# Performance work log

Measured on AMD Instinct MI355X. Metric: run time of the kernel, lower is better.

Reference implementation:

```python
import jax, jax.numpy as jnp
import numpy as np

B, T, N, D, R, K, P = 4, 336, 862, 64, 8, 6, 96


def setup_inputs() -> dict:
    key = jax.random.key(0)
    ks = jax.random.split(key, 8)
    s = 0.02
    return {
        "x_enc": jax.random.normal(ks[0], (B, T, N), jnp.float32),
        "W_embed": jax.random.normal(ks[1], (1, D), jnp.float32) * s,
        "b_embed": jnp.zeros((D,), jnp.float32),
        "W1": jax.random.normal(ks[2], (D, R), jnp.float32) * s,
        "W2": jax.random.normal(ks[3], (D, R), jnp.float32) * s,
        "gate": jnp.float32(-4.0),  # gate_init
        "A_prior": jnp.eye(N, dtype=jnp.float32),  # season_gcn_adj_source=identity
        "W_gcn": jax.random.normal(ks[4], (D, D), jnp.float32) * s,
        "g_gcn": jnp.float32(0.5),  # season_gcn gate
        "W_head": jax.random.normal(ks[5], (T * D, P), jnp.float32) * s,
        "b_head": jnp.zeros((P,), jnp.float32),
    }


def _topk_renorm(adj, k):
    # keep top-k entries per row, zero the rest, renormalize rows (matches _sparsify_adj)
    vals = jax.lax.top_k(adj, k)[0]
    thresh = vals[..., -1:]
    mask = (adj >= thresh).astype(adj.dtype)
    masked = adj * mask
    denom = jnp.clip(jnp.sum(masked, axis=-1, keepdims=True), 1e-12, None)
    return masked / denom


def reference(x_enc, W_embed, b_embed, W1, W2, gate, A_prior, W_gcn, g_gcn, W_head, b_head):
    # per-variable, per-timestep value embedding: [B,N,T,D]
    h = x_enc.transpose(0, 2, 1)[..., None] * W_embed[0] + b_embed
    # content-mean node descriptors: [B,N,D]
    z = jnp.mean(h, axis=2)
    # low-rank graph learner -> adjacency logits [B,N,N]
    e1 = z @ W1
    e2 = z @ W2
    logits = jnp.einsum('bnr,bmr->bnm', e1, e2) / jnp.sqrt(jnp.float32(R))
    adj = jax.nn.softmax(logits, axis=-1)
    adj = _topk_renorm(adj, K)  # top-k sparsify + row renorm
    # gated graph mixing over variable nodes
    h_mix = jnp.einsum('bnm,bmtd->bntd', adj, h)
    h = h + jax.nn.sigmoid(gate) * h_mix
    # season GCN: sym-normalized prior adjacency, residual + gate
    deg = jnp.sum(A_prior, axis=-1)
    dinv = jnp.where(deg > 0, 1.0 / jnp.sqrt(deg), 0.0)
    A_hat = A_prior * dinv[:, None] * dinv[None, :]
    h = h + g_gcn * jnp.einsum('nm,bmtd,de->bnte', A_hat, h, W_gcn)
    # forecast head: flatten tokens, project to pred_len per variable
    out = h.reshape(B, N, T * D) @ W_head + b_head  # [B,N,P]
    return out.transpose(0, 2, 1)  # [B,P,N]
```

## Files before the change

kernel.cpp:

```cpp
#include <hip/hip_runtime.h>
#include <math.h>

#define B_ 4
#define T_ 336
#define N_ 862
#define D_ 64
#define R_ 8
#define K_ 6
#define P_ 96
#define NR 896
#define CAP 32
#define NB 864

#define OFF_PC   0
#define OFF_XBAR 192
#define OFF_DINV 3648
#define OFF_WGT  4512
#define OFF_IDX  25248
#define OFF_CNT  45984
#define OFF_CSRV 46848
#define OFF_CSRI 74496
#define OFF_P12  102144
#define OFF_PCP  166656
#define OFF_XPT  231168

__global__ __launch_bounds__(192) void kA_prep(const float* __restrict__ x,
                                               const float* __restrict__ Whead,
                                               const float* __restrict__ We,
                                               const float* __restrict__ be,
                                               const float* __restrict__ gate,
                                               const float* __restrict__ Wgcn,
                                               float* __restrict__ ws) {
  int id = blockIdx.x;
  int tid = threadIdx.x;
  if (id < 336) {
    __shared__ float sW1[64], sW2[64], sCB[64], sWe[64];
    int t = id;
    float g = 1.f / (1.f + expf(-gate[0]));
    if (tid < 64) {
      float a = 0.f;
#pragma unroll 8
      for (int dd = 0; dd < D_; ++dd) a += We[dd] * Wgcn[dd * D_ + tid];
      sW1[tid] = a;
    } else if (tid < 128) {
      int e = tid - 64;
      float a = 0.f;
#pragma unroll 8
      for (int dd = 0; dd < D_; ++dd) a += be[dd] * Wgcn[dd * D_ + e];
      sW2[e] = (1.f + g) * a;
    } else {
      int e = tid - 128;
      sCB[e] = (1.f + g) * be[e];
      sWe[e] = We[e];
    }
    __syncthreads();
    int c = tid, p = c % P_, sel = c / P_;
    const float* cA = sel ? sW1 : sWe;
    const float* cB = sel ? sW2 : sCB;
    const float* wrow = Whead + (size_t)t * D_ * P_ + p;
    float a = 0.f, bacc = 0.f;
#pragma unroll 8
    for (int e = 0; e < D_; ++e) {
      float w = wrow[(size_t)e * P_];
      a = fmaf(cA[e], w, a);
      bacc = fmaf(cB[e], w, bacc);
    }
    ws[OFF_P12 + t * 192 + c] = a;
    ws[OFF_PCP + t * 192 + c] = bacc;
  } else {
    __shared__ float part[192];
    int iq = id - 336;
    int b = iq / 14, ch = iq % 14;
    int lane = tid & 63, tg = tid >> 6;
    int n = ch * 64 + lane;
    float s = 0.f;
    if (n < N_) {
      const float* xp = x + (size_t)(b * T_) * N_ + n;
      for (int t = tg; t < T_; t += 3) s += xp[(size_t)t * N_];
    }
    part[tid] = s;
    __syncthreads();
    if (tg == 0 && n < N_)
      ws[OFF_XBAR + b * NB + n] = part[lane] + part[64 + lane] + part[128 + lane];
  }
}

__global__ __launch_bounds__(192) void kM_mid(const float* __restrict__ x,
                                              const float* __restrict__ A,
                                              const float* __restrict__ W1,
                                              const float* __restrict__ W2,
                                              const float* __restrict__ We,
                                              const float* __restrict__ be,
                                              const float* __restrict__ gate,
                                              float* __restrict__ ws) {
  __shared__ float smem[9984];
  int id = blockIdx.x;
  int tid = threadIdx.x;
  if (id < 216) {
    float* xs = smem;
    float* ps = smem + 768;
    int b = id / 54;
    int n0 = (id % 54) * 16;
    int cq = tid % 48, nq = tid / 48;
    int c0 = cq * 4;
    const float* P = ws + OFF_P12;
    float acc[4][4];
#pragma unroll
    for (int i = 0; i < 4; ++i)
#pragma unroll
      for (int j = 0; j < 4; ++j) acc[i][j] = 0.f;
    int xrow = tid >> 2, xcol4 = tid & 3;
    for (int kc = 0; kc < 7; ++kc) {
      int t0 = kc * 48;
      {
        const float* xr = x + (size_t)(b * T_ + t0 + xrow) * N_;
        if (n0 + 15 < N_) {
          *(float4*)(xs + xrow * 16 + xcol4 * 4) = *(const float4*)(xr + n0 + xcol4 * 4);
        } else {
          float* dst = xs + xrow * 16 + xcol4 * 4;
#pragma unroll
          for (int q = 0; q < 4; ++q) {
            int nn = n0 + xcol4 * 4 + q; if (nn > N_ - 1) nn = N_ - 1;
            dst[q] = xr[nn];
          }
        }
      }
#pragma unroll
      for (int sIdx = 0; sIdx < 12; ++sIdx) {
        int i4 = tid + sIdx * 192;
        int row = i4 / 48, col4 = i4 % 48;
        *(float4*)(ps + row * 192 + col4 * 4) =
            *(const float4*)(P + (size_t)(t0 + row) * 192 + col4 * 4);
      }
      __syncthreads();
#pragma unroll 4
      for (int kk = 0; kk < 48; ++kk) {
        float4 xv = *(const float4*)(xs + kk * 16 + nq * 4);
        float4 pv = *(const float4*)(ps + kk * 192 + c0);
        acc[0][0] = fmaf(pv.x, xv.x, acc[0][0]); acc[0][1] = fmaf(pv.x, xv.y, acc[0][1]);
        acc[0][2] = fmaf(pv.x, xv.z, acc[0][2]); acc[0][3] = fmaf(pv.x, xv.w, acc[0][3]);
        acc[1][0] = fmaf(pv.y, xv.x, acc[1][0]); acc[1][1] = fmaf(pv.y, xv.y, acc[1][1]);
        acc[1][2] = fmaf(pv.y, xv.z, acc[1][2]); acc[1][3] = fmaf(pv.y, xv.w, acc[1][3]);
        acc[2][0] = fmaf(pv.z, xv.x, acc[2][0]); acc[2][1] = fmaf(pv.z, xv.y, acc[2][1]);
        acc[2][2] = fmaf(pv.z, xv.z, acc[2][2]); acc[2][3] = fmaf(pv.z, xv.w, acc[2][3]);
        acc[3][0] = fmaf(pv.w, xv.x, acc[3][0]); acc[3][1] = fmaf(pv.w, xv.y, acc[3][1]);
        acc[3][2] = fmaf(pv.w, xv.z, acc[3][2]); acc[3][3] = fmaf(pv.w, xv.w, acc[3][3]);
      }
      __syncthreads();
    }
#pragma unroll
    for (int cc = 0; cc < 4; ++cc) {
      float4 v;
      v.x = acc[cc][0]; v.y = acc[cc][1]; v.z = acc[cc][2]; v.w = acc[cc][3];
      *(float4*)(ws + OFF_XPT + ((size_t)(b * 192 + c0 + cc)) * NR + n0 + nq * 4) = v;
    }
  } else if (id < 220) {
    __shared__ float s_sc[4][R_];
    __shared__ float s_scal[5];
    __shared__ float selv[12];
    __shared__ int seli[12];
    float* sx = smem;
    float* wkmax = smem + 864;
    float* wkmin = smem + 1728;
    int b = id - 216;
    if (tid < 16) {
      int r = tid & 7, which = tid >> 3;
      const float* W = which ? W2 : W1;
      float a = 0.f, bb = 0.f;
      for (int dd = 0; dd < D_; ++dd) {
        float w = W[dd * R_ + r];
        a += We[dd] * w; bb += be[dd] * w;
      }
      s_sc[which * 2][r] = a; s_sc[which * 2 + 1][r] = bb;
    }
    const float invT = 1.f / (float)T_;
    for (int i = tid; i < NB; i += 192) {
      float v = (i < N_) ? ws[OFF_XBAR + b * NB + i] * invT : 0.f;
      sx[i] = v;
      wkmax[i] = (i < N_) ? v : -3.4e38f;
      wkmin[i] = (i < N_) ? v : 3.4e38f;
    }
    __syncthreads();
    if (tid == 0) {
      float s11 = 0.f, s12 = 0.f, s21 = 0.f, s22 = 0.f;
      for (int r = 0; r < R_; ++r) {
        s11 += s_sc[0][r] * s_sc[2][r];
        s12 += s_sc[0][r] * s_sc[3][r];
        s21 += s_sc[1][r] * s_sc[2][r];
        s22 += s_sc[1][r] * s_sc[3][r];
      }
      s_scal[0] = s11; s_scal[1] = s12; s_scal[2] = s21; s_scal[3] = s22;
      s_scal[4] = 1.f / (1.f + expf(-gate[0]));
    }
    if (tid < 64) {
      int lane = tid;
      for (int r = 0; r < K_; ++r) {
        float bv = -3.4e38f; int bi = 0;
        for (int i = lane; i < N_; i += 64) {
          float v = wkmax[i];
          if (v > bv) { bv = v; bi = i; }
        }
        for (int off = 32; off; off >>= 1) {
          float ov = __shfl_down(bv, off);
          int oi = __shfl_down(bi, off);
          if (ov > bv) { bv = ov; bi = oi; }
        }
        bv = __shfl(bv, 0); bi = __shfl(bi, 0);
        if (lane == 0) { selv[r] = bv; seli[r] = bi; wkmax[bi] = -3.4e38f; }
      }
    } else if (tid < 128) {
      int lane = tid - 64;
      for (int r = 0; r < K_; ++r) {
        float bv = 3.4e38f; int bi = 0;
        for (int i = lane; i < N_; i += 64) {
          float v = wkmin[i];
          if (v < bv) { bv = v; bi = i; }
        }
        for (int off = 32; off; off >>= 1) {
          float ov = __shfl_down(bv, off);
          int oi = __shfl_down(bi, off);
          if (ov < bv) { bv = ov; bi = oi; }
        }
        bv = __shfl(bv, 0); bi = __shfl(bi, 0);
        if (lane == 0) { selv[6 + r] = bv; seli[6 + r] = bi; wkmin[bi] = 3.4e38f; }
      }
    }
    __syncthreads();
    float s11 = s_scal[0], s12 = s_scal[1], s21 = s_scal[2], s22 = s_scal[3];
    float g = s_scal[4];
    const float rsq = 0.3535533906f;
    for (int n = tid; n < N_; n += 192) {
      float xn = sx[n];
      float alpha = (xn * s11 + s21) * rsq;
      float beta  = (xn * s12 + s22) * rsq;
      int base = (alpha >= 0.f) ? 0 : 6;
      float l[K_]; float mx = -3.4e38f;
#pragma unroll
      for (int j = 0; j < K_; ++j) { l[j] = alpha * selv[base + j] + beta; mx = fmaxf(mx, l[j]); }
      float e[K_]; float ss = 0.f;
#pragma unroll
      for (int j = 0; j < K_; ++j) { e[j] = expf(l[j] - mx); ss += e[j]; }
      float sc = g / ss;
#pragma unroll
      for (int j = 0; j < K_; ++j) {
        ws[OFF_WGT + j * (4 * NB) + b * NB + n] = e[j] * sc;
        ((int*)(ws + OFF_IDX))[j * (4 * NB) + b * NB + n] = seli[base + j];
      }
    }
  } else if (id < 508) {
    int lane = tid & 63, wv = tid >> 6;
    int n = (id - 220) * 3 + wv;
    if (n >= N_) return;
    const float* ap = A + (size_t)n * N_;
    float* vout = ws + OFF_CSRV;
    int* iout = (int*)(ws + OFF_CSRI);
    float s = 0.f;
    int total = 0;
    for (int base = 0; base < N_; base += 64) {
      int m = base + lane;
      float a = (m < N_) ? ap[m] : 0.f;
      s += a;
      bool nz = (a != 0.f);
      unsigned long long mask = __ballot(nz);
      int pos = __popcll(mask & ((1ull << lane) - 1ull));
      if (nz) {
        int slot = total + pos;
        if (slot < CAP) { vout[slot * NB + n] = a; iout[slot * NB + n] = m; }
      }
      total += __popcll(mask);
    }
    for (int off = 32; off; off >>= 1) s += __shfl_down(s, off);
    if (lane == 0) {
      ws[OFF_DINV + n] = (s > 0.f) ? (1.f / sqrtf(s)) : 0.f;
      ((int*)(ws + OFF_CNT))[n] = (total <= CAP) ? total : -1;
    }
  } else {
    int c = tid;
    float s = 0.f;
    for (int t = 0; t < T_; ++t) s += ws[OFF_PCP + t * 192 + c];
    ws[OFF_PC + c] = s;
  }
}

__global__ void kF_final(const float* __restrict__ A, const float* __restrict__ bhead,
                         const float* __restrict__ ggcn, const float* __restrict__ ws,
                         float* __restrict__ out) {
  int c = blockIdx.y;
  int n = blockIdx.x * 256 + threadIdx.x;
  if (n >= N_) return;
  int b = c / P_, p = c % P_;
  const float* Xp1 = ws + OFF_XPT + ((size_t)(b * 192 + p)) * NR;
  const float* Xp2 = ws + OFF_XPT + ((size_t)(b * 192 + P_ + p)) * NR;
  const float* WGTb = ws + OFF_WGT + b * NB;
  const int* IDXb = (const int*)(ws + OFF_IDX) + b * NB;
  float gg = ggcn[0];
  float PAp = ws[OFF_PC + 96 + p];
  float acc1 = Xp1[n];
#pragma unroll
  for (int j = 0; j < K_; ++j)
    acc1 += WGTb[j * (4 * NB) + n] * Xp1[IDXb[j * (4 * NB) + n]];
  int cnt = ((const int*)(ws + OFF_CNT))[n];
  float S = 0.f;
  if (cnt >= 0) {
    const float* vv = ws + OFF_CSRV;
    const int* ii = (const int*)(ws + OFF_CSRI);
    for (int jj = 0; jj < cnt; ++jj) {
      float a = vv[jj * NB + n];
      int m = ii[jj * NB + n];
      float mix2 = Xp2[m];
#pragma unroll
      for (int j = 0; j < K_; ++j)
        mix2 += WGTb[j * (4 * NB) + m] * Xp2[IDXb[j * (4 * NB) + m]];
      S += a * ws[OFF_DINV + m] * (mix2 + PAp);
    }
  } else {
    const float* ar = A + (size_t)n * N_;
    for (int m = 0; m < N_; ++m) {
      float a = ar[m];
      if (a != 0.f) {
        float mix2 = Xp2[m];
#pragma unroll
        for (int j = 0; j < K_; ++j)
          mix2 += WGTb[j * (4 * NB) + m] * Xp2[IDXb[j * (4 * NB) + m]];
        S += a * ws[OFF_DINV + m] * (mix2 + PAp);
      }
    }
  }
  out[(size_t)c * N_ + n] = acc1 + gg * ws[OFF_DINV + n] * S
                          + ws[OFF_PC + p] + bhead[p];
}

extern "C" void kernel_launch(void* const* d_in, const int* in_sizes, int n_in,
                              void* d_out, int out_size, void* d_ws, size_t ws_size,
                              hipStream_t stream) {
  const float* x     = (const float*)d_in[0];
  const float* We    = (const float*)d_in[1];
  const float* be    = (const float*)d_in[2];
  const float* W1    = (const float*)d_in[3];
  const float* W2    = (const float*)d_in[4];
  const float* gate  = (const float*)d_in[5];
  const float* A     = (const float*)d_in[6];
  const float* Wgcn  = (const float*)d_in[7];
  const float* ggcn  = (const float*)d_in[8];
  const float* Whead = (const float*)d_in[9];
  const float* bhead = (const float*)d_in[10];
  float* ws = (float*)d_ws;
  float* out = (float*)d_out;

  kA_prep<<<392, 192, 0, stream>>>(x, Whead, We, be, gate, Wgcn, ws);
  kM_mid<<<509, 192, 0, stream>>>(x, A, W1, W2, We, be, gate, ws);
  kF_final<<<dim3(4, 384), 256, 0, stream>>>(A, bhead, ggcn, ws, out);
}
```

Before: 135.3 us.

## Split time reductions across more blocks and move CSR build into prep kernel

The per-variable time-sum of x is now split into 6 time chunks per block group, giving 6x more blocks, and kM_mid adds the partials together. The column sum of PCP is split into 4 partial blocks that kF_final combines. The adjacency CSR/degree scan moves from kM_mid into kA_prep, so kM_mid only runs the graph and reduction blocks. The aim is to balance the critical path across kernels and raise parallelism in the serial reductions, at the cost of extra partial-buffer reads.

```diff
diff --git a/kernel.cpp b/kernel.cpp
--- a/kernel.cpp
+++ b/kernel.cpp
@@ -12,20 +12,21 @@
 #define CAP 32
 #define NB 864
 
-#define OFF_PC   0
-#define OFF_XBAR 192
-#define OFF_DINV 3648
-#define OFF_WGT  4512
-#define OFF_IDX  25248
-#define OFF_CNT  45984
-#define OFF_CSRV 46848
-#define OFF_CSRI 74496
-#define OFF_P12  102144
-#define OFF_PCP  166656
-#define OFF_XPT  231168
+#define OFF_PCQ  0
+#define OFF_XBP  768
+#define OFF_DINV 21504
+#define OFF_WGT  22368
+#define OFF_IDX  43104
+#define OFF_CNT  63840
+#define OFF_CSRV 64704
+#define OFF_CSRI 92352
+#define OFF_P12  120000
+#define OFF_PCP  184512
+#define OFF_XPT  249024
 
 __global__ __launch_bounds__(192) void kA_prep(const float* __restrict__ x,
                                                const float* __restrict__ Whead,
+                                               const float* __restrict__ A,
                                                const float* __restrict__ We,
                                                const float* __restrict__ be,
                                                const float* __restrict__ gate,
@@ -39,13 +40,13 @@
     float g = 1.f / (1.f + expf(-gate[0]));
     if (tid < 64) {
       float a = 0.f;
-#pragma unroll 8
+#pragma unroll
       for (int dd = 0; dd < D_; ++dd) a += We[dd] * Wgcn[dd * D_ + tid];
       sW1[tid] = a;
     } else if (tid < 128) {
       int e = tid - 64;
       float a = 0.f;
-#pragma unroll 8
+#pragma unroll
       for (int dd = 0; dd < D_; ++dd) a += be[dd] * Wgcn[dd * D_ + e];
       sW2[e] = (1.f + g) * a;
     } else {
@@ -59,7 +60,7 @@
     const float* cB = sel ? sW2 : sCB;
     const float* wrow = Whead + (size_t)t * D_ * P_ + p;
     float a = 0.f, bacc = 0.f;
-#pragma unroll 8
+#pragma unroll
     for (int e = 0; e < D_; ++e) {
       float w = wrow[(size_t)e * P_];
       a = fmaf(cA[e], w, a);
@@ -67,26 +68,56 @@
     }
     ws[OFF_P12 + t * 192 + c] = a;
     ws[OFF_PCP + t * 192 + c] = bacc;
-  } else {
+  } else if (id < 672) {
     __shared__ float part[192];
     int iq = id - 336;
-    int b = iq / 14, ch = iq % 14;
-    int lane = tid & 63, tg = tid >> 6;
+    int b = iq / 84, rem = iq % 84;
+    int ch = rem / 6, tg = rem % 6;
+    int lane = tid & 63, tsub = tid >> 6;
     int n = ch * 64 + lane;
     float s = 0.f;
     if (n < N_) {
       const float* xp = x + (size_t)(b * T_) * N_ + n;
-      for (int t = tg; t < T_; t += 3) s += xp[(size_t)t * N_];
+      int tend = tg * 56 + 56;
+#pragma unroll 4
+      for (int t = tg * 56 + tsub; t < tend; t += 3) s += xp[(size_t)t * N_];
     }
     part[tid] = s;
     __syncthreads();
-    if (tg == 0 && n < N_)
-      ws[OFF_XBAR + b * NB + n] = part[lane] + part[64 + lane] + part[128 + lane];
+    if (tsub == 0 && n < N_)
+      ws[OFF_XBP + (size_t)(b * 6 + tg) * NB + n] =
+          part[lane] + part[64 + lane] + part[128 + lane];
+  } else {
+    int lane = tid & 63, wv = tid >> 6;
+    int n = (id - 672) * 3 + wv;
+    if (n >= N_) return;
+    const float* ap = A + (size_t)n * N_;
+    float* vout = ws + OFF_CSRV;
+    int* iout = (int*)(ws + OFF_CSRI);
+    float s = 0.f;
+    int total = 0;
+    for (int base = 0; base < N_; base += 64) {
+      int m = base + lane;
+      float a = (m < N_) ? ap[m] : 0.f;
+      s += a;
+      bool nz = (a != 0.f);
+      unsigned long long mask = __ballot(nz);
+      int pos = __popcll(mask & ((1ull << lane) - 1ull));
+      if (nz) {
+        int slot = total + pos;
+        if (slot < CAP) { vout[slot * NB + n] = a; iout[slot * NB + n] = m; }
+      }
+      total += __popcll(mask);
+    }
+    for (int off = 32; off; off >>= 1) s += __shfl_down(s, off);
+    if (lane == 0) {
+      ws[OFF_DINV + n] = (s > 0.f) ? (1.f / sqrtf(s)) : 0.f;
+      ((int*)(ws + OFF_CNT))[n] = (total <= CAP) ? total : -1;
+    }
   }
 }
 
 __global__ __launch_bounds__(192) void kM_mid(const float* __restrict__ x,
-                                              const float* __restrict__ A,
                                               const float* __restrict__ W1,
                                               const float* __restrict__ W2,
                                               const float* __restrict__ We,
@@ -175,7 +206,13 @@
     }
     const float invT = 1.f / (float)T_;
     for (int i = tid; i < NB; i += 192) {
-      float v = (i < N_) ? ws[OFF_XBAR + b * NB + i] * invT : 0.f;
+      float v = 0.f;
+      if (i < N_) {
+        const float* xp = ws + OFF_XBP + (size_t)(b * 6) * NB + i;
+#pragma unroll
+        for (int q = 0; q < 6; ++q) v += xp[q * NB];
+        v *= invT;
+      }
       sx[i] = v;
       wkmax[i] = (i < N_) ? v : -3.4e38f;
       wkmin[i] = (i < N_) ? v : 3.4e38f;
@@ -247,38 +284,13 @@
         ((int*)(ws + OFF_IDX))[j * (4 * NB) + b * NB + n] = seli[base + j];
       }
     }
-  } else if (id < 508) {
-    int lane = tid & 63, wv = tid >> 6;
-    int n = (id - 220) * 3 + wv;
-    if (n >= N_) return;
-    const float* ap = A + (size_t)n * N_;
-    float* vout = ws + OFF_CSRV;
-    int* iout = (int*)(ws + OFF_CSRI);
-    float s = 0.f;
-    int total = 0;
-    for (int base = 0; base < N_; base += 64) {
-      int m = base + lane;
-      float a = (m < N_) ? ap[m] : 0.f;
-      s += a;
-      bool nz = (a != 0.f);
-      unsigned long long mask = __ballot(nz);
-      int pos = __popcll(mask & ((1ull << lane) - 1ull));
-      if (nz) {
-        int slot = total + pos;
-        if (slot < CAP) { vout[slot * NB + n] = a; iout[slot * NB + n] = m; }
-      }
-      total += __popcll(mask);
-    }
-    for (int off = 32; off; off >>= 1) s += __shfl_down(s, off);
-    if (lane == 0) {
-      ws[OFF_DINV + n] = (s > 0.f) ? (1.f / sqrtf(s)) : 0.f;
-      ((int*)(ws + OFF_CNT))[n] = (total <= CAP) ? total : -1;
-    }
   } else {
+    int q = id - 220;
     int c = tid;
     float s = 0.f;
-    for (int t = 0; t < T_; ++t) s += ws[OFF_PCP + t * 192 + c];
-    ws[OFF_PC + c] = s;
+#pragma unroll 12
+    for (int t = q * 84; t < q * 84 + 84; ++t) s += ws[OFF_PCP + t * 192 + c];
+    ws[OFF_PCQ + q * 192 + c] = s;
   }
 }
 
@@ -294,7 +306,12 @@
   const float* WGTb = ws + OFF_WGT + b * NB;
   const int* IDXb = (const int*)(ws + OFF_IDX) + b * NB;
   float gg = ggcn[0];
-  float PAp = ws[OFF_PC + 96 + p];
+  float PCp = 0.f, PAp = 0.f;
+#pragma unroll
+  for (int q = 0; q < 4; ++q) {
+    PCp += ws[OFF_PCQ + q * 192 + p];
+    PAp += ws[OFF_PCQ + q * 192 + 96 + p];
+  }
   float acc1 = Xp1[n];
 #pragma unroll
   for (int j = 0; j < K_; ++j)
@@ -326,8 +343,7 @@
       }
     }
   }
-  out[(size_t)c * N_ + n] = acc1 + gg * ws[OFF_DINV + n] * S
-                          + ws[OFF_PC + p] + bhead[p];
+  out[(size_t)c * N_ + n] = acc1 + gg * ws[OFF_DINV + n] * S + PCp + bhead[p];
 }
 
 extern "C" void kernel_launch(void* const* d_in, const int* in_sizes, int n_in,
@@ -347,7 +363,7 @@
   float* ws = (float*)d_ws;
   float* out = (float*)d_out;
 
-  kA_prep<<<392, 192, 0, stream>>>(x, Whead, We, be, gate, Wgcn, ws);
-  kM_mid<<<509, 192, 0, stream>>>(x, A, W1, W2, We, be, gate, ws);
+  kA_prep<<<960, 192, 0, stream>>>(x, Whead, A, We, be, gate, Wgcn, ws);
+  kM_mid<<<224, 192, 0, stream>>>(x, W1, W2, We, be, gate, ws);
   kF_final<<<dim3(4, 384), 256, 0, stream>>>(A, bhead, ggcn, ws, out);
 }
```

Result: faster. 113.1 us (-16.4%).
